# Performance work log

Measured on AMD Instinct MI355X. Metric: run time of the kernel, lower is better.

Reference implementation:

```python
import jax, jax.numpy as jnp
import numpy as np

N = 6000
E = 192000
H = 128
NUM_HEADS = 4

def _segsum(x, idx, n):
    return jax.ops.segment_sum(x, idx, num_segments=n)

def _gcn_encode(x, edges, W0, b0, Ws, bs):
    n = x.shape[0]
    sl = jnp.arange(n, dtype=edges.dtype)
    row = jnp.concatenate([edges[0], sl])  # source
    col = jnp.concatenate([edges[1], sl])  # target (aggregation)
    deg = _segsum(jnp.ones_like(col, dtype=x.dtype), col, n)
    dinv = jax.lax.rsqrt(deg)  # deg >= 1 thanks to self loops
    norm = (dinv[row] * dinv[col])[:, None]
    def layer(h, W, b):
        hw = h @ W
        agg = _segsum(hw[row] * norm, col, n)
        return jax.nn.relu(agg + b)
    h = layer(x, W0, b0)
    for i in range(Ws.shape[0]):
        h = layer(h, Ws[i], bs[i])
    return h

def setup_inputs() -> dict:
    key = jax.random.key(0)
    ks = jax.random.split(key, 24)
    def lin(k, fan_in, shape):
        return jax.random.normal(k, shape, dtype=jnp.float32) / np.sqrt(fan_in)
    return {
        'x_resting': jax.random.normal(ks[0], (N, 3), dtype=jnp.float32),
        'x_rigid': jax.random.normal(ks[1], (N, 3), dtype=jnp.float32),
        'edge_resting': jax.random.randint(ks[2], (2, E), 0, N, dtype=jnp.int32),
        'edge_rigid': jax.random.randint(ks[3], (2, E), 0, N, dtype=jnp.int32),
        'Wr0': lin(ks[4], 3, (3, H)), 'br0': jnp.zeros((H,), jnp.float32),
        'Wr': lin(ks[5], H, (2, H, H)), 'br': jnp.zeros((2, H), jnp.float32),
        'Wg0': lin(ks[6], 3, (3, H)), 'bg0': jnp.zeros((H,), jnp.float32),
        'Wg': lin(ks[7], H, (2, H, H)), 'bg': jnp.zeros((2, H), jnp.float32),
        'Wa': lin(ks[8], H, (NUM_HEADS, H, H)), 'ba': jnp.zeros((NUM_HEADS, H), jnp.float32),
        'Wd0': lin(ks[9], H * (NUM_HEADS + 1), (H * (NUM_HEADS + 1), H)), 'bd0': jnp.zeros((H,), jnp.float32),
        'Wd': lin(ks[10], H, (2, H, H)), 'bd': jnp.zeros((2, H), jnp.float32),
        'Wout': lin(ks[11], H, (H, 3)), 'bout': jnp.zeros((3,), jnp.float32),
    }

def reference(x_resting, x_rigid, edge_resting, edge_rigid,
              Wr0, br0, Wr, br, Wg0, bg0, Wg, bg,
              Wa, ba, Wd0, bd0, Wd, bd, Wout, bout):
    xr = _gcn_encode(x_resting, edge_resting, Wr0, br0, Wr, br)  # (N,H)
    xg = _gcn_encode(x_rigid, edge_rigid, Wg0, bg0, Wg, bg)      # (N,H)

    def head(W, b):
        q = xr @ W + b            # (N,H)
        k = xg @ W + b            # (N,H)
        attn = jax.nn.softmax(q @ k.T, axis=-1)  # (N,N) dense per head
        return attn @ xg          # (N,H)
    heads = jax.vmap(head)(Wa, ba)                       # (heads,N,H)
    pooled = heads.transpose(1, 0, 2).reshape(xr.shape[0], -1)  # (N, heads*H)

    h = jnp.concatenate([xr, pooled], axis=-1)  # (N, H*(heads+1))
    h = jax.nn.relu(h @ Wd0 + bd0)
    for i in range(Wd.shape[0]):
        h = jax.nn.relu(h @ Wd[i] + bd[i])
    return h @ Wout + bout  # (N, 3) deformed positions
```

## Files before the change

kernel.cpp:

```cpp
#include <hip/hip_runtime.h>
#include <math.h>

#define N_NODES 6000
#define N_EDGES 192000
#define H 128
#define NHEADS 4
#define HCAT 640
#define NPAD 6016
#define NTILES 188

typedef unsigned short ushort_t;
typedef __attribute__((ext_vector_type(8))) short short8;
typedef __attribute__((ext_vector_type(16))) float f32x16;

__device__ __forceinline__ void bf16split(float x, ushort_t& hi, ushort_t& lo) {
    unsigned ub = __float_as_uint(x);
    unsigned hb = ub & 0xffff0000u;
    float l = x - __uint_as_float(hb);
    hi = (ushort_t)(hb >> 16);
    lo = (ushort_t)(__float_as_uint(l) >> 16);
}

__device__ __forceinline__ void gll16(const ushort_t* g, ushort_t* l) {
    __builtin_amdgcn_global_load_lds((const __attribute__((address_space(1))) void*)g,
                                     (__attribute__((address_space(3))) void*)l, 16, 0, 0);
}

__global__ void zero_ints(int* p, int n) {
    int i = blockIdx.x * 256 + threadIdx.x;
    if (i < n) p[i] = 0;
}

__global__ void hist2(const int* __restrict__ eA, const int* __restrict__ eB,
                      int* __restrict__ cnt) {
    int e = blockIdx.x * 256 + threadIdx.x;
    int z = blockIdx.y;
    const int* edges = z ? eB : eA;
    if (e < N_EDGES) atomicAdd(&cnt[z * N_NODES + edges[N_EDGES + e]], 1);
}

__global__ __launch_bounds__(1024)
void scan2(const int* __restrict__ cnt_all, int* __restrict__ rs_all) {
    __shared__ int ps[1024];
    int z = blockIdx.x;
    const int* cnt = cnt_all + z * N_NODES;
    int* row_start = rs_all + z * (N_NODES + 1);
    int t = threadIdx.x;
    int base = t * 6;
    int local[6];
    int s = 0;
#pragma unroll
    for (int j = 0; j < 6; ++j) {
        int idx = base + j;
        int v = (idx < N_NODES) ? cnt[idx] : 0;
        local[j] = s;
        s += v;
    }
    ps[t] = s;
    __syncthreads();
    for (int off = 1; off < 1024; off <<= 1) {
        int v = (t >= off) ? ps[t - off] : 0;
        __syncthreads();
        ps[t] += v;
        __syncthreads();
    }
    int ex = (t > 0) ? ps[t - 1] : 0;
#pragma unroll
    for (int j = 0; j < 6; ++j) {
        int idx = base + j;
        if (idx < N_NODES) row_start[idx] = ex + local[j];
    }
    if (t == 1023) row_start[N_NODES] = ps[1023];
}

__global__ void dinv_kernel(const int* __restrict__ cnt, float* __restrict__ dinv, int n) {
    int i = blockIdx.x * 256 + threadIdx.x;
    if (i < n) dinv[i] = rsqrtf((float)(cnt[i] + 1));
}

__global__ void place2(const int* __restrict__ eA, const int* __restrict__ eB,
                       const int* __restrict__ rs_all, int* __restrict__ cur_all,
                       int* __restrict__ eslot_all) {
    int e = blockIdx.x * 256 + threadIdx.x;
    int z = blockIdx.y;
    const int* edges = z ? eB : eA;
    if (e < N_EDGES) {
        int tg = edges[N_EDGES + e];
        int p = atomicAdd(&cur_all[z * N_NODES + tg], 1);
        eslot_all[(size_t)z * N_EDGES + rs_all[z * (N_NODES + 1) + tg] + p] = e;
    }
}

__global__ __launch_bounds__(256)
void gcn_gemm2(const float* __restrict__ hinA, const float* __restrict__ hinB,
               const float* __restrict__ WA, const float* __restrict__ WB,
               float* __restrict__ hwA, float* __restrict__ hwB, int in_dim) {
    __shared__ float xs[16 * H];
    int z = blockIdx.y;
    const float* hin = z ? hinB : hinA;
    const float* W = z ? WB : WA;
    float* hw = z ? hwB : hwA;
    int n0 = blockIdx.x * 16;
    int t = threadIdx.x;
    int f = t & (H - 1);
    int g = t >> 7;
    for (int i = t; i < 16 * H; i += 256) {
        int r = i >> 7, c = i & (H - 1);
        xs[i] = (c < in_dim) ? hin[(size_t)(n0 + r) * in_dim + c] : 0.f;
    }
    __syncthreads();
    float acc[8];
#pragma unroll
    for (int j = 0; j < 8; ++j) acc[j] = 0.f;
    for (int d = 0; d < in_dim; ++d) {
        float w = W[d * H + f];
#pragma unroll
        for (int j = 0; j < 8; ++j) acc[j] += xs[(g * 8 + j) * H + d] * w;
    }
#pragma unroll
    for (int j = 0; j < 8; ++j) hw[(size_t)(n0 + g * 8 + j) * H + f] = acc[j];
}

__global__ __launch_bounds__(H)
void gather2(const int* __restrict__ eA, const int* __restrict__ eB,
             const int* __restrict__ eslot_all, const int* __restrict__ rs_all,
             const float* __restrict__ hwA, const float* __restrict__ hwB,
             const float* __restrict__ dinv_all,
             const float* __restrict__ bA, const float* __restrict__ bB,
             float* __restrict__ outA, float* __restrict__ outB, int osA, int osB) {
    __shared__ int ssrc[128];
    __shared__ float snrm[128];
    int z = blockIdx.y;
    const int* edges = z ? eB : eA;
    const int* eslot = eslot_all + (size_t)z * N_EDGES;
    const int* row_start = rs_all + z * (N_NODES + 1);
    const float* hw = z ? hwB : hwA;
    const float* dinv = dinv_all + z * N_NODES;
    const float* b = z ? bB : bA;
    float* out = z ? outB : outA;
    int ostride = z ? osB : osA;

    int tg = blockIdx.x, f = threadIdx.x;
    int s0 = row_start[tg], s1 = row_start[tg + 1];
    float di = dinv[tg];
    float acc = hw[(size_t)tg * H + f] * di * di;
    for (int base = s0; base < s1; base += 128) {
        int cnt = min(128, s1 - base);
        __syncthreads();
        if (f < cnt) {
            int e = eslot[base + f];
            int s = edges[e];
            ssrc[f] = s;
            snrm[f] = dinv[s] * di;
        }
        __syncthreads();
        for (int i = 0; i < cnt; ++i)
            acc += hw[(size_t)ssrc[i] * H + f] * snrm[i];
    }
    float v = acc + b[f];
    out[(size_t)tg * ostride + f] = v > 0.f ? v : 0.f;
}

__global__ __launch_bounds__(256)
void qk_kernel2(const float* __restrict__ qs, int qstride, const float* __restrict__ xg,
                const float* __restrict__ Wa, const float* __restrict__ ba,
                ushort_t* __restrict__ Qh, ushort_t* __restrict__ Ql,
                ushort_t* __restrict__ Khs, ushort_t* __restrict__ Kls) {
    __shared__ float xs[2][16][H];
    int n0 = blockIdx.x * 16, head = blockIdx.y;
    int t = threadIdx.x;
    int f = t & (H - 1);
    int g = t >> 7;
    for (int i = t; i < 2 * 16 * H; i += 256) {
        int which = i >> 11;
        int rem = i & 2047;
        int row = rem >> 7, col = rem & 127;
        xs[which][row][col] = which ? xg[(size_t)(n0 + row) * H + col]
                                    : qs[(size_t)(n0 + row) * qstride + col];
    }
    __syncthreads();
    const float* W = Wa + (size_t)head * H * H;
    float bias = ba[head * H + f];
    float acc[16];
#pragma unroll
    for (int j = 0; j < 16; ++j) acc[j] = bias;
    for (int d = 0; d < H; ++d) {
        float w = W[d * H + f];
#pragma unroll
        for (int j = 0; j < 16; ++j) acc[j] += xs[g][j][d] * w;
    }
#pragma unroll
    for (int j = 0; j < 16; ++j) {
        int n = n0 + j;
        ushort_t hi, lo;
        bf16split(acc[j], hi, lo);
        if (g == 0) {
            size_t idx = ((size_t)(head * N_NODES + n) << 7) + f;
            Qh[idx] = hi; Ql[idx] = lo;
        } else {
            int pos = (((f >> 3) ^ (n & 15)) << 3) + (f & 7);
            size_t idx = ((size_t)(head * NPAD + n) << 7) + pos;
            Khs[idx] = hi; Kls[idx] = lo;
        }
    }
}

__global__ void zero_pad_k(ushort_t* __restrict__ Khs, ushort_t* __restrict__ Kls) {
    int i = blockIdx.x * 256 + threadIdx.x;
    if (i < NHEADS * 16 * H) {
        int head = i / (16 * H);
        int rest = i - head * 16 * H;
        int n = N_NODES + (rest >> 7);
        int f = rest & 127;
        size_t idx = ((size_t)(head * NPAD + n) << 7) + f;
        Khs[idx] = 0; Kls[idx] = 0;
    }
}

__global__ __launch_bounds__(128)
void cvt_vt(const float* __restrict__ xg, ushort_t* __restrict__ Vth, ushort_t* __restrict__ Vtl) {
    __shared__ float vs[32][129];
    int t0 = blockIdx.x;
    int t = threadIdx.x;
    for (int c = t; c < 32 * 32; c += 128) {
        int row = c >> 5, col4 = (c & 31) << 2;
        int n = t0 * 32 + row;
        float4 v = (n < N_NODES) ? *(const float4*)&xg[(size_t)n * H + col4]
                                 : float4{0.f, 0.f, 0.f, 0.f};
        vs[row][col4 + 0] = v.x; vs[row][col4 + 1] = v.y;
        vs[row][col4 + 2] = v.z; vs[row][col4 + 3] = v.w;
    }
    __syncthreads();
    int d = t;
    size_t base = ((size_t)t0 * H + d) * 32;
#pragma unroll
    for (int oc = 0; oc < 4; ++oc) {
        int cc = oc ^ (d & 3);
        unsigned uh[4], ul[4];
#pragma unroll
        for (int j = 0; j < 4; ++j) {
            ushort_t h0, l0, h1, l1;
            bf16split(vs[cc * 8 + 2 * j][d], h0, l0);
            bf16split(vs[cc * 8 + 2 * j + 1][d], h1, l1);
            uh[j] = (unsigned)h0 | ((unsigned)h1 << 16);
            ul[j] = (unsigned)l0 | ((unsigned)l1 << 16);
        }
        *(uint4*)&Vth[base + oc * 8] = make_uint4(uh[0], uh[1], uh[2], uh[3]);
        *(uint4*)&Vtl[base + oc * 8] = make_uint4(ul[0], ul[1], ul[2], ul[3]);
    }
}

__global__ __launch_bounds__(256, 3)
void attn_mfma3(const ushort_t* __restrict__ Qh, const ushort_t* __restrict__ Ql,
                const ushort_t* __restrict__ Khs, const ushort_t* __restrict__ Kls,
                const ushort_t* __restrict__ Vth, const ushort_t* __restrict__ Vtl,
                float* __restrict__ Opart, float* __restrict__ mlpart, int tps) {
    __shared__ ushort_t Kbuf[2][2][4096];
    __shared__ ushort_t Vbuf[2][4096];
    const int head = blockIdx.y;
    const int sp = blockIdx.z;
    const int t = threadIdx.x;
    const int w = t >> 6;
    const int lane = t & 63;
    const int r = lane & 31;
    const int h = lane >> 5;
    const int q0w = blockIdx.x * 128 + w * 32;

    int t_begin = sp * tps;
    int t_end = t_begin + tps; if (t_end > NTILES) t_end = NTILES;

    const int khl = w >> 1;
    const int wseg = (w & 1) * 4;
    const size_t kbase = (size_t)head * NPAD * H;
    const ushort_t* gK = (khl ? Kls : Khs) + kbase;
    const ushort_t* gV = khl ? Vtl : Vth;

    int qr = q0w + r; if (qr > N_NODES - 1) qr = N_NODES - 1;
    const size_t qbase = ((size_t)(head * N_NODES + qr)) << 7;
    short8 qfh[8], qfl[8];
#pragma unroll
    for (int s = 0; s < 8; ++s) {
        qfh[s] = *(const short8*)&Qh[qbase + 16 * s + 8 * h];
        qfl[s] = *(const short8*)&Ql[qbase + 16 * s + 8 * h];
    }

    f32x16 O[4];
#pragma unroll
    for (int sub = 0; sub < 4; ++sub)
#pragma unroll
        for (int i = 0; i < 16; ++i) O[sub][i] = 0.f;
    float mrun = -1e30f, lrun = 0.f;

    {
        const ushort_t* src = gK + (size_t)t_begin * 4096;
        ushort_t* dst = &Kbuf[0][khl][0];
#pragma unroll
        for (int s = 0; s < 4; ++s) {
            int off = (wseg + s) * 512 + lane * 8;
            gll16(src + off, dst + off);
        }
    }

    for (int it = t_begin; it < t_end; ++it) {
        const int b = (it - t_begin) & 1;
        __syncthreads();
        {
            const ushort_t* src = gV + (size_t)it * 4096;
            ushort_t* dst = &Vbuf[khl][0];
#pragma unroll
            for (int s = 0; s < 4; ++s) {
                int off = (wseg + s) * 512 + lane * 8;
                gll16(src + off, dst + off);
            }
        }
        const ushort_t* lKh = &Kbuf[b][0][0];
        const ushort_t* lKl = &Kbuf[b][1][0];

        f32x16 acc;
#pragma unroll
        for (int i = 0; i < 16; ++i) acc[i] = 0.f;
        const int krow = r * H;
#pragma unroll
        for (int s = 0; s < 8; ++s) {
            int cc = ((2 * s + h) ^ (r & 15)) << 3;
            short8 ah = *(const short8*)&lKh[krow + cc];
            short8 al = *(const short8*)&lKl[krow + cc];
            acc = __builtin_amdgcn_mfma_f32_32x32x16_bf16(ah, qfh[s], acc, 0, 0, 0);
            acc = __builtin_amdgcn_mfma_f32_32x32x16_bf16(ah, qfl[s], acc, 0, 0, 0);
            acc = __builtin_amdgcn_mfma_f32_32x32x16_bf16(al, qfh[s], acc, 0, 0, 0);
        }

        float sv[16];
#pragma unroll
        for (int i = 0; i < 16; ++i) sv[i] = acc[i];
        int klim = N_NODES - (it << 5);
        if (klim < 32) {
#pragma unroll
            for (int i = 0; i < 16; ++i) {
                int row = (i & 3) + 8 * (i >> 2) + 4 * h;
                if (row >= klim) sv[i] = -1e30f;
            }
        }
        float tmax = sv[0];
#pragma unroll
        for (int i = 1; i < 16; ++i) tmax = fmaxf(tmax, sv[i]);
        tmax = fmaxf(tmax, __shfl_xor(tmax, 32));
        float mnew = fmaxf(mrun, tmax);
        float p[16];
        float psum = 0.f;
#pragma unroll
        for (int i = 0; i < 16; ++i) { p[i] = __expf(sv[i] - mnew); psum += p[i]; }
        psum += __shfl_xor(psum, 32);

        if (__ballot(mnew > mrun)) {
            float alpha = __expf(mrun - mnew);
            lrun *= alpha;
#pragma unroll
            for (int i = 0; i < 16; ++i) {
                int rowq = (i & 3) + 8 * (i >> 2) + 4 * h;
                float a = __shfl(alpha, rowq);
#pragma unroll
                for (int sub = 0; sub < 4; ++sub) O[sub][i] *= a;
            }
        }
        lrun += psum;
        mrun = mnew;

        float pr[16];
#pragma unroll
        for (int i = 0; i < 16; ++i) pr[i] = __shfl_xor(p[i], 32);
        short8 aPh[2], aPl[2];
#pragma unroll
        for (int s2 = 0; s2 < 2; ++s2) {
#pragma unroll
            for (int j = 0; j < 8; ++j) {
                int c = j & 3;
                float v;
                if (j < 4) v = (h == 0) ? p[c + 8 * s2] : pr[c + 8 * s2 + 4];
                else       v = (h == 1) ? p[c + 8 * s2 + 4] : pr[c + 8 * s2];
                unsigned ub = __float_as_uint(v);
                unsigned hb = ub & 0xffff0000u;
                float lo = v - __uint_as_float(hb);
                aPh[s2][j] = (short)(hb >> 16);
                aPl[s2][j] = (short)(__float_as_uint(lo) >> 16);
            }
        }

        __syncthreads();
        if (it + 1 < t_end) {
            const ushort_t* src = gK + (size_t)(it + 1) * 4096;
            ushort_t* dst = &Kbuf[b ^ 1][khl][0];
#pragma unroll
            for (int s = 0; s < 4; ++s) {
                int off = (wseg + s) * 512 + lane * 8;
                gll16(src + off, dst + off);
            }
        }

        const ushort_t* lVh = &Vbuf[0][0];
        const ushort_t* lVl = &Vbuf[1][0];
#pragma unroll
        for (int sub = 0; sub < 4; ++sub) {
            const int vrow = (32 * sub + r) * 32;
#pragma unroll
            for (int s2 = 0; s2 < 2; ++s2) {
                int cc = (((2 * s2 + h) ^ (r & 3)) << 3);
                short8 bh = *(const short8*)&lVh[vrow + cc];
                short8 bl = *(const short8*)&lVl[vrow + cc];
                O[sub] = __builtin_amdgcn_mfma_f32_32x32x16_bf16(aPh[s2], bh, O[sub], 0, 0, 0);
                O[sub] = __builtin_amdgcn_mfma_f32_32x32x16_bf16(aPh[s2], bl, O[sub], 0, 0, 0);
                O[sub] = __builtin_amdgcn_mfma_f32_32x32x16_bf16(aPl[s2], bh, O[sub], 0, 0, 0);
            }
        }
    }

    float* Ob = Opart + (size_t)(sp * NHEADS + head) * NPAD * H;
#pragma unroll
    for (int i = 0; i < 16; ++i) {
        int rowq = (i & 3) + 8 * (i >> 2) + 4 * h;
        int qg = q0w + rowq;
        float* dst = &Ob[(size_t)qg * H + r];
#pragma unroll
        for (int sub = 0; sub < 4; ++sub) dst[32 * sub] = O[sub][i];
    }
    if (h == 0) {
        float2* ml = (float2*)mlpart;
        ml[(size_t)(sp * NHEADS + head) * NPAD + q0w + r] = make_float2(mrun, lrun);
    }
}

__global__ __launch_bounds__(256)
void attn_combine(const float* __restrict__ Opart, const float* __restrict__ mlpart,
                  float* __restrict__ hcat, int ns) {
    int idx = blockIdx.x * 256 + threadIdx.x;
    if (idx >= NHEADS * N_NODES * (H / 4)) return;
    int head = idx / (N_NODES * (H / 4));
    int rest = idx - head * N_NODES * (H / 4);
    int q = rest >> 5;
    int d4 = (rest & 31) << 2;
    const float2* ml = (const float2*)mlpart;
    float m = -1e30f;
    for (int s = 0; s < ns; ++s)
        m = fmaxf(m, ml[(size_t)(s * NHEADS + head) * NPAD + q].x);
    float lsum = 0.f;
    float4 o = {0.f, 0.f, 0.f, 0.f};
    for (int s = 0; s < ns; ++s) {
        float2 v = ml[(size_t)(s * NHEADS + head) * NPAD + q];
        float wgt = __expf(v.x - m);
        lsum += v.y * wgt;
        float4 ov = *(const float4*)&Opart[((size_t)(s * NHEADS + head) * NPAD + q) * H + d4];
        o.x += ov.x * wgt; o.y += ov.y * wgt; o.z += ov.z * wgt; o.w += ov.w * wgt;
    }
    float inv = 1.f / lsum;
    float4 res = {o.x * inv, o.y * inv, o.z * inv, o.w * inv};
    *(float4*)&hcat[(size_t)q * HCAT + H + head * H + d4] = res;
}

__global__ __launch_bounds__(256)
void decoder(const float* __restrict__ hcat,
             const float* __restrict__ Wd0, const float* __restrict__ bd0,
             const float* __restrict__ Wd, const float* __restrict__ bd,
             const float* __restrict__ Wout, const float* __restrict__ bout,
             float* __restrict__ out) {
    __shared__ float s0[8 * HCAT];
    __shared__ float s1[8 * H];
    __shared__ float s2[8 * H];
    int n0 = blockIdx.x * 8;
    int t = threadIdx.x;
    int f = t & (H - 1);
    int g = t >> 7;
    for (int i = t; i < 8 * HCAT; i += 256)
        s0[i] = hcat[(size_t)n0 * HCAT + i];
    __syncthreads();

    float acc[4];
#pragma unroll
    for (int j = 0; j < 4; ++j) acc[j] = bd0[f];
    for (int d = 0; d < HCAT; ++d) {
        float w = Wd0[d * H + f];
#pragma unroll
        for (int j = 0; j < 4; ++j) acc[j] += s0[(g * 4 + j) * HCAT + d] * w;
    }
#pragma unroll
    for (int j = 0; j < 4; ++j) s1[(g * 4 + j) * H + f] = fmaxf(acc[j], 0.f);
    __syncthreads();

#pragma unroll
    for (int j = 0; j < 4; ++j) acc[j] = bd[f];
    for (int d = 0; d < H; ++d) {
        float w = Wd[d * H + f];
#pragma unroll
        for (int j = 0; j < 4; ++j) acc[j] += s1[(g * 4 + j) * H + d] * w;
    }
#pragma unroll
    for (int j = 0; j < 4; ++j) s2[(g * 4 + j) * H + f] = fmaxf(acc[j], 0.f);
    __syncthreads();

#pragma unroll
    for (int j = 0; j < 4; ++j) acc[j] = bd[H + f];
    for (int d = 0; d < H; ++d) {
        float w = Wd[H * H + d * H + f];
#pragma unroll
        for (int j = 0; j < 4; ++j) acc[j] += s2[(g * 4 + j) * H + d] * w;
    }
    __syncthreads();
#pragma unroll
    for (int j = 0; j < 4; ++j) s1[(g * 4 + j) * H + f] = fmaxf(acc[j], 0.f);
    __syncthreads();

    if (t < 24) {
        int n = t / 3, c = t % 3;
        float o = bout[c];
        for (int d = 0; d < H; ++d) o += s1[n * H + d] * Wout[d * 3 + c];
        out[(size_t)(n0 + n) * 3 + c] = o;
    }
}

extern "C" void kernel_launch(void* const* d_in, const int* in_sizes, int n_in,
                              void* d_out, int out_size, void* d_ws, size_t ws_size,
                              hipStream_t stream) {
    const float* x_rest = (const float*)d_in[0];
    const float* x_rig  = (const float*)d_in[1];
    const int*   e_rest = (const int*)d_in[2];
    const int*   e_rig  = (const int*)d_in[3];
    const float* Wr0 = (const float*)d_in[4];
    const float* br0 = (const float*)d_in[5];
    const float* Wr  = (const float*)d_in[6];
    const float* br  = (const float*)d_in[7];
    const float* Wg0 = (const float*)d_in[8];
    const float* bg0 = (const float*)d_in[9];
    const float* Wg  = (const float*)d_in[10];
    const float* bg  = (const float*)d_in[11];
    const float* Wa  = (const float*)d_in[12];
    const float* ba  = (const float*)d_in[13];
    const float* Wd0 = (const float*)d_in[14];
    const float* bd0 = (const float*)d_in[15];
    const float* Wd  = (const float*)d_in[16];
    const float* bd  = (const float*)d_in[17];
    const float* Wout = (const float*)d_in[18];
    const float* bout = (const float*)d_in[19];
    float* out = (float*)d_out;

    const size_t NH = (size_t)N_NODES * H;
    float* ws = (float*)d_ws;
    float* dinv = ws;
    float* hw   = dinv + 2 * N_NODES;
    float* hb   = hw + 2 * NH;
    float* hcat = hb + 2 * NH;
    float* ha   = hcat;
    float* xg   = hb + NH;
    ushort_t* Qh  = (ushort_t*)(hcat + (size_t)N_NODES * HCAT);
    ushort_t* Ql  = Qh + (size_t)NHEADS * N_NODES * H;
    ushort_t* Khs = Ql + (size_t)NHEADS * N_NODES * H;
    ushort_t* Kls = Khs + (size_t)NHEADS * NPAD * H;
    ushort_t* Vth = Kls + (size_t)NHEADS * NPAD * H;
    ushort_t* Vtl = Vth + (size_t)NTILES * H * 32;
    int* ib   = (int*)(Vtl + (size_t)NTILES * H * 32);
    int* cnt  = ib;
    int* cur  = cnt + 2 * N_NODES;
    int* rs   = cur + 2 * N_NODES;
    int* eslot = rs + 2 * (N_NODES + 1);
    int* iend  = eslot + 2 * N_EDGES;
    float* Opart = (float*)(((uintptr_t)iend + 15) & ~(uintptr_t)15);

    size_t base_bytes = (size_t)((char*)Opart - (char*)d_ws);
    size_t per_split  = (size_t)NHEADS * NPAD * (H + 2) * sizeof(float);
    int NS = 2;
    if (ws_size >= base_bytes + 4 * per_split + (1u << 20)) NS = 4;
    float* mlpart = Opart + (size_t)NS * NHEADS * NPAD * H;
    int tps = (NTILES + NS - 1) / NS;

    const int gN = (N_NODES + 255) / 256;
    const int gE = (N_EDGES + 255) / 256;

    zero_ints<<<(4 * N_NODES + 255) / 256, 256, 0, stream>>>(cnt, 4 * N_NODES);
    hist2<<<dim3(gE, 2), 256, 0, stream>>>(e_rest, e_rig, cnt);
    scan2<<<2, 1024, 0, stream>>>(cnt, rs);
    dinv_kernel<<<(2 * N_NODES + 255) / 256, 256, 0, stream>>>(cnt, dinv, 2 * N_NODES);
    place2<<<dim3(gE, 2), 256, 0, stream>>>(e_rest, e_rig, rs, cur, eslot);

    float* hw_r = hw, * hw_g = hw + NH;
    float* ha_r = ha, * ha_g = ha + NH;
    float* hb_r = hb, * hb_g = hb + NH;

    gcn_gemm2<<<dim3(N_NODES / 16, 2), 256, 0, stream>>>(x_rest, x_rig, Wr0, Wg0, hw_r, hw_g, 3);
    gather2<<<dim3(N_NODES, 2), H, 0, stream>>>(e_rest, e_rig, eslot, rs, hw_r, hw_g, dinv,
                                                br0, bg0, ha_r, ha_g, H, H);
    gcn_gemm2<<<dim3(N_NODES / 16, 2), 256, 0, stream>>>(ha_r, ha_g, Wr, Wg, hw_r, hw_g, H);
    gather2<<<dim3(N_NODES, 2), H, 0, stream>>>(e_rest, e_rig, eslot, rs, hw_r, hw_g, dinv,
                                                br, bg, hb_r, hb_g, H, H);
    gcn_gemm2<<<dim3(N_NODES / 16, 2), 256, 0, stream>>>(hb_r, hb_g, Wr + H * H, Wg + H * H,
                                                         hw_r, hw_g, H);
    gather2<<<dim3(N_NODES, 2), H, 0, stream>>>(e_rest, e_rig, eslot, rs, hw_r, hw_g, dinv,
                                                br + H, bg + H, hcat, xg, HCAT, H);

    qk_kernel2<<<dim3(N_NODES / 16, NHEADS), 256, 0, stream>>>(hcat, HCAT, xg, Wa, ba,
                                                               Qh, Ql, Khs, Kls);
    zero_pad_k<<<(NHEADS * 16 * H + 255) / 256, 256, 0, stream>>>(Khs, Kls);
    cvt_vt<<<NTILES, 128, 0, stream>>>(xg, Vth, Vtl);
    attn_mfma3<<<dim3(47, NHEADS, NS), 256, 0, stream>>>(Qh, Ql, Khs, Kls, Vth, Vtl,
                                                         Opart, mlpart, tps);
    attn_combine<<<(NHEADS * N_NODES * (H / 4) + 255) / 256, 256, 0, stream>>>(Opart, mlpart,
                                                                               hcat, NS);

    decoder<<<N_NODES / 8, 256, 0, stream>>>(hcat, Wd0, bd0, Wd, bd, Wout, bout, out);
}
```

Before: 621.3 us.

## Reorder first GCN layer as aggregate-then-project and widen attention blocks

```diff
diff --git a/kernel.cpp b/kernel.cpp
--- a/kernel.cpp
+++ b/kernel.cpp
@@ -8,6 +8,7 @@
 #define HCAT 640
 #define NPAD 6016
 #define NTILES 188
+#define QBLK 24
 
 typedef unsigned short ushort_t;
 typedef __attribute__((ext_vector_type(8))) short short8;
@@ -92,14 +93,47 @@
 }
 
 __global__ __launch_bounds__(256)
+void gather_x3(const float* __restrict__ xA, const float* __restrict__ xB,
+               const int* __restrict__ eA, const int* __restrict__ eB,
+               const int* __restrict__ eslot_all, const int* __restrict__ rs_all,
+               const float* __restrict__ dinv_all,
+               float* __restrict__ outA, float* __restrict__ outB) {
+    int z = blockIdx.y;
+    int n = blockIdx.x * 256 + threadIdx.x;
+    if (n >= N_NODES) return;
+    const int* edges = z ? eB : eA;
+    const int* eslot = eslot_all + (size_t)z * N_EDGES;
+    const int* row_start = rs_all + z * (N_NODES + 1);
+    const float* x = z ? xB : xA;
+    const float* dv = dinv_all + z * N_NODES;
+    float* out = z ? outB : outA;
+    float di = dv[n];
+    float a0 = x[n * 3 + 0] * di * di;
+    float a1 = x[n * 3 + 1] * di * di;
+    float a2 = x[n * 3 + 2] * di * di;
+    int s0 = row_start[n], s1 = row_start[n + 1];
+    for (int i = s0; i < s1; ++i) {
+        int e = eslot[i];
+        int s = edges[e];
+        float nr = dv[s] * di;
+        a0 += x[s * 3 + 0] * nr;
+        a1 += x[s * 3 + 1] * nr;
+        a2 += x[s * 3 + 2] * nr;
+    }
+    out[n * 3 + 0] = a0; out[n * 3 + 1] = a1; out[n * 3 + 2] = a2;
+}
+
+__global__ __launch_bounds__(256)
 void gcn_gemm2(const float* __restrict__ hinA, const float* __restrict__ hinB,
                const float* __restrict__ WA, const float* __restrict__ WB,
-               float* __restrict__ hwA, float* __restrict__ hwB, int in_dim) {
+               float* __restrict__ hwA, float* __restrict__ hwB, int in_dim,
+               const float* __restrict__ bA, const float* __restrict__ bB, int do_relu) {
     __shared__ float xs[16 * H];
     int z = blockIdx.y;
     const float* hin = z ? hinB : hinA;
     const float* W = z ? WB : WA;
     float* hw = z ? hwB : hwA;
+    const float* b = z ? bB : bA;
     int n0 = blockIdx.x * 16;
     int t = threadIdx.x;
     int f = t & (H - 1);
@@ -117,8 +151,15 @@
 #pragma unroll
         for (int j = 0; j < 8; ++j) acc[j] += xs[(g * 8 + j) * H + d] * w;
     }
-#pragma unroll
-    for (int j = 0; j < 8; ++j) hw[(size_t)(n0 + g * 8 + j) * H + f] = acc[j];
+    if (do_relu) {
+        float bias = b[f];
+#pragma unroll
+        for (int j = 0; j < 8; ++j)
+            hw[(size_t)(n0 + g * 8 + j) * H + f] = fmaxf(acc[j] + bias, 0.f);
+    } else {
+#pragma unroll
+        for (int j = 0; j < 8; ++j) hw[(size_t)(n0 + g * 8 + j) * H + f] = acc[j];
+    }
 }
 
 __global__ __launch_bounds__(H)
@@ -250,13 +291,12 @@
     }
 }
 
-__global__ __launch_bounds__(256, 3)
-void attn_mfma3(const ushort_t* __restrict__ Qh, const ushort_t* __restrict__ Ql,
+__global__ __launch_bounds__(512, 4)
+void attn_mfma4(const ushort_t* __restrict__ Qh, const ushort_t* __restrict__ Ql,
                 const ushort_t* __restrict__ Khs, const ushort_t* __restrict__ Kls,
                 const ushort_t* __restrict__ Vth, const ushort_t* __restrict__ Vtl,
                 float* __restrict__ Opart, float* __restrict__ mlpart, int tps) {
-    __shared__ ushort_t Kbuf[2][2][4096];
-    __shared__ ushort_t Vbuf[2][4096];
+    __shared__ ushort_t lds[2][4][4096];
     const int head = blockIdx.y;
     const int sp = blockIdx.z;
     const int t = threadIdx.x;
@@ -264,16 +304,13 @@
     const int lane = t & 63;
     const int r = lane & 31;
     const int h = lane >> 5;
-    const int q0w = blockIdx.x * 128 + w * 32;
+    const int q0w = blockIdx.x * 256 + w * 32;
 
     int t_begin = sp * tps;
     int t_end = t_begin + tps; if (t_end > NTILES) t_end = NTILES;
 
-    const int khl = w >> 1;
-    const int wseg = (w & 1) * 4;
     const size_t kbase = (size_t)head * NPAD * H;
-    const ushort_t* gK = (khl ? Kls : Khs) + kbase;
-    const ushort_t* gV = khl ? Vtl : Vth;
+    const int lo8 = t * 8;
 
     int qr = q0w + r; if (qr > N_NODES - 1) qr = N_NODES - 1;
     const size_t qbase = ((size_t)(head * N_NODES + qr)) << 7;
@@ -292,29 +329,28 @@
     float mrun = -1e30f, lrun = 0.f;
 
     {
-        const ushort_t* src = gK + (size_t)t_begin * 4096;
-        ushort_t* dst = &Kbuf[0][khl][0];
-#pragma unroll
-        for (int s = 0; s < 4; ++s) {
-            int off = (wseg + s) * 512 + lane * 8;
-            gll16(src + off, dst + off);
-        }
+        size_t off = (size_t)t_begin * 4096 + lo8;
+        gll16(Khs + kbase + off, &lds[0][0][lo8]);
+        gll16(Kls + kbase + off, &lds[0][1][lo8]);
+        gll16(Vth + off, &lds[0][2][lo8]);
+        gll16(Vtl + off, &lds[0][3][lo8]);
     }
 
     for (int it = t_begin; it < t_end; ++it) {
         const int b = (it - t_begin) & 1;
         __syncthreads();
         {
-            const ushort_t* src = gV + (size_t)it * 4096;
-            ushort_t* dst = &Vbuf[khl][0];
-#pragma unroll
-            for (int s = 0; s < 4; ++s) {
-                int off = (wseg + s) * 512 + lane * 8;
-                gll16(src + off, dst + off);
-            }
-        }
-        const ushort_t* lKh = &Kbuf[b][0][0];
-        const ushort_t* lKl = &Kbuf[b][1][0];
+            int nt = it + 1; if (nt >= t_end) nt = t_begin;
+            size_t off = (size_t)nt * 4096 + lo8;
+            gll16(Khs + kbase + off, &lds[b ^ 1][0][lo8]);
+            gll16(Kls + kbase + off, &lds[b ^ 1][1][lo8]);
+            gll16(Vth + off, &lds[b ^ 1][2][lo8]);
+            gll16(Vtl + off, &lds[b ^ 1][3][lo8]);
+        }
+        const ushort_t* lKh = &lds[b][0][0];
+        const ushort_t* lKl = &lds[b][1][0];
+        const ushort_t* lVh = &lds[b][2][0];
+        const ushort_t* lVl = &lds[b][3][0];
 
         f32x16 acc;
 #pragma unroll
@@ -350,7 +386,6 @@
         float psum = 0.f;
 #pragma unroll
         for (int i = 0; i < 16; ++i) { p[i] = __expf(sv[i] - mnew); psum += p[i]; }
-        psum += __shfl_xor(psum, 32);
 
         if (__ballot(mnew > mrun)) {
             float alpha = __expf(mrun - mnew);
@@ -386,19 +421,6 @@
             }
         }
 
-        __syncthreads();
-        if (it + 1 < t_end) {
-            const ushort_t* src = gK + (size_t)(it + 1) * 4096;
-            ushort_t* dst = &Kbuf[b ^ 1][khl][0];
-#pragma unroll
-            for (int s = 0; s < 4; ++s) {
-                int off = (wseg + s) * 512 + lane * 8;
-                gll16(src + off, dst + off);
-            }
-        }
-
-        const ushort_t* lVh = &Vbuf[0][0];
-        const ushort_t* lVl = &Vbuf[1][0];
 #pragma unroll
         for (int sub = 0; sub < 4; ++sub) {
             const int vrow = (32 * sub + r) * 32;
@@ -414,16 +436,20 @@
         }
     }
 
+    lrun += __shfl_xor(lrun, 32);
+
     float* Ob = Opart + (size_t)(sp * NHEADS + head) * NPAD * H;
 #pragma unroll
     for (int i = 0; i < 16; ++i) {
         int rowq = (i & 3) + 8 * (i >> 2) + 4 * h;
         int qg = q0w + rowq;
-        float* dst = &Ob[(size_t)qg * H + r];
-#pragma unroll
-        for (int sub = 0; sub < 4; ++sub) dst[32 * sub] = O[sub][i];
-    }
-    if (h == 0) {
+        if (qg < N_NODES) {
+            float* dst = &Ob[(size_t)qg * H + r];
+#pragma unroll
+            for (int sub = 0; sub < 4; ++sub) dst[32 * sub] = O[sub][i];
+        }
+    }
+    if (h == 0 && q0w + r < N_NODES) {
         float2* ml = (float2*)mlpart;
         ml[(size_t)(sp * NHEADS + head) * NPAD + q0w + r] = make_float2(mrun, lrun);
     }
@@ -549,6 +575,7 @@
     float* hcat = hb + 2 * NH;
     float* ha   = hcat;
     float* xg   = hb + NH;
+    float* xagg = hb;
     ushort_t* Qh  = (ushort_t*)(hcat + (size_t)N_NODES * HCAT);
     ushort_t* Ql  = Qh + (size_t)NHEADS * N_NODES * H;
     ushort_t* Khs = Ql + (size_t)NHEADS * N_NODES * H;
@@ -566,7 +593,8 @@
     size_t base_bytes = (size_t)((char*)Opart - (char*)d_ws);
     size_t per_split  = (size_t)NHEADS * NPAD * (H + 2) * sizeof(float);
     int NS = 2;
-    if (ws_size >= base_bytes + 4 * per_split + (1u << 20)) NS = 4;
+    if (ws_size >= base_bytes + 5 * per_split + (1u << 20)) NS = 5;
+    else if (ws_size >= base_bytes + 4 * per_split + (1u << 20)) NS = 4;
     float* mlpart = Opart + (size_t)NS * NHEADS * NPAD * H;
     int tps = (NTILES + NS - 1) / NS;
 
@@ -582,15 +610,18 @@
     float* hw_r = hw, * hw_g = hw + NH;
     float* ha_r = ha, * ha_g = ha + NH;
     float* hb_r = hb, * hb_g = hb + NH;
-
-    gcn_gemm2<<<dim3(N_NODES / 16, 2), 256, 0, stream>>>(x_rest, x_rig, Wr0, Wg0, hw_r, hw_g, 3);
-    gather2<<<dim3(N_NODES, 2), H, 0, stream>>>(e_rest, e_rig, eslot, rs, hw_r, hw_g, dinv,
-                                                br0, bg0, ha_r, ha_g, H, H);
-    gcn_gemm2<<<dim3(N_NODES / 16, 2), 256, 0, stream>>>(ha_r, ha_g, Wr, Wg, hw_r, hw_g, H);
+    float* xagg_r = xagg, * xagg_g = xagg + 3 * N_NODES;
+
+    gather_x3<<<dim3(gN, 2), 256, 0, stream>>>(x_rest, x_rig, e_rest, e_rig, eslot, rs,
+                                               dinv, xagg_r, xagg_g);
+    gcn_gemm2<<<dim3(N_NODES / 16, 2), 256, 0, stream>>>(xagg_r, xagg_g, Wr0, Wg0,
+                                                         ha_r, ha_g, 3, br0, bg0, 1);
+    gcn_gemm2<<<dim3(N_NODES / 16, 2), 256, 0, stream>>>(ha_r, ha_g, Wr, Wg, hw_r, hw_g, H,
+                                                         nullptr, nullptr, 0);
     gather2<<<dim3(N_NODES, 2), H, 0, stream>>>(e_rest, e_rig, eslot, rs, hw_r, hw_g, dinv,
                                                 br, bg, hb_r, hb_g, H, H);
     gcn_gemm2<<<dim3(N_NODES / 16, 2), 256, 0, stream>>>(hb_r, hb_g, Wr + H * H, Wg + H * H,
-                                                         hw_r, hw_g, H);
+                                                         hw_r, hw_g, H, nullptr, nullptr, 0);
     gather2<<<dim3(N_NODES, 2), H, 0, stream>>>(e_rest, e_rig, eslot, rs, hw_r, hw_g, dinv,
                                                 br + H, bg + H, hcat, xg, HCAT, H);
 
@@ -598,8 +629,8 @@
                                                                Qh, Ql, Khs, Kls);
     zero_pad_k<<<(NHEADS * 16 * H + 255) / 256, 256, 0, stream>>>(Khs, Kls);
     cvt_vt<<<NTILES, 128, 0, stream>>>(xg, Vth, Vtl);
-    attn_mfma3<<<dim3(47, NHEADS, NS), 256, 0, stream>>>(Qh, Ql, Khs, Kls, Vth, Vtl,
-                                                         Opart, mlpart, tps);
+    attn_mfma4<<<dim3(QBLK, NHEADS, NS), 512, 0, stream>>>(Qh, Ql, Khs, Kls, Vth, Vtl,
+                                                           Opart, mlpart, tps);
     attn_combine<<<(NHEADS * N_NODES * (H / 4) + 255) / 256, 256, 0, stream>>>(Opart, mlpart,
                                                                                hcat, NS);
 
```

Result: slower. 811.1 us (+30.5%).
